# Performance work log

Hardware: AMD Instinct MI355X
Metric: run time of the kernel (lower is better)

Reference implementation:

```python
import jax, jax.numpy as jnp
import numpy as np

B, N, C, H = 4, 4096, 1024, 16
D = C // H


def setup_inputs() -> dict:
    key = jax.random.key(0)
    ks = jax.random.split(key, 15)
    s = 0.02
    f = lambda k, shp: jax.random.normal(k, shp, dtype=jnp.float32) * s
    return {
        "x": f(ks[0], (B, N, C)),
        "qkv_w": f(ks[1], (C, 3 * C)),
        "qkv_b": f(ks[2], (3 * C,)),
        "out_w": f(ks[3], (C, C)),
        "out_b": f(ks[4], (C,)),
        # NB: original code dynamically re-creates position_bias as (1, N, H, H)
        # because q/k/v are never transposed to (B,H,N,D); attention runs over heads.
        "pos_bias": f(ks[5], (1, N, H, H)),
        "conv_w": f(ks[6], (C, C)),
        "conv_b": f(ks[7], (C,)),
        "pw_w": f(ks[8], (C, C, 1)),   # Conv1d kernel_size=1: (out, in, k)
        "pw_b": f(ks[9], (C,)),
        "dw_w": f(ks[10], (C, 1, 3)),  # depthwise Conv1d groups=C: (out, in/groups=1, k)
        "dw_b": f(ks[11], (C,)),
        "tok_w": f(ks[12], (C, C)),
        "tok_b": f(ks[13], (C,)),
    }


def reference(x, qkv_w, qkv_b, out_w, out_b, pos_bias,
              conv_w, conv_b, pw_w, pw_b, dw_w, dw_b, tok_w, tok_b):
    b, n, c = x.shape
    h = pos_bias.shape[2]
    d = c // h
    scale = d ** (-0.5)

    # ---- attention branch (faithful to source: heads axis is attended over) ----
    qkv = (x @ qkv_w + qkv_b).reshape(b, n, h, 3 * d)
    q, k, v = jnp.split(qkv, 3, axis=-1)  # each (B, N, H, D)
    scores = jnp.einsum("bnhd,bngd->bnhg", q, k) * scale + pos_bias  # (B, N, H, H)
    attn_w = jax.nn.softmax(scores, axis=-1)
    attn = jnp.einsum("bnhg,bngd->bnhd", attn_w, v).reshape(b, n, c)
    attn = attn @ out_w + out_b

    # ---- convolutional branch ----
    xc = x @ conv_w + conv_b            # (B, N, C)
    xc = xc.transpose(0, 2, 1)          # (B, C, N)
    dn = ("NCH", "OIH", "NCH")
    xc = jax.lax.conv_general_dilated(xc, pw_w, (1,), [(0, 0)],
                                      dimension_numbers=dn) + pw_b[None, :, None]
    xc = jax.lax.conv_general_dilated(xc, dw_w, (1,), [(1, 1)],
                                      dimension_numbers=dn,
                                      feature_group_count=c) + dw_b[None, :, None]
    xc = xc.transpose(0, 2, 1) @ tok_w + tok_b  # (B, N, C)

    return attn + xc
```

## Files before the change

### kernel.cpp

```cpp
#include <hip/hip_runtime.h>
#include <hip/hip_bf16.h>


typedef __attribute__((ext_vector_type(8))) short sh8;
typedef __attribute__((ext_vector_type(4))) float f4;

__device__ __forceinline__ float bf2f(short s) {
  unsigned u = ((unsigned)(unsigned short)s) << 16;
  return __builtin_bit_cast(float, u);
}
__device__ __forceinline__ short f2bf(float f) {
  return __builtin_bit_cast(short, __float2bfloat16(f));
}
__device__ __forceinline__ void g2l16(const void* g, void* l) {
  __builtin_amdgcn_global_load_lds(
      (const __attribute__((address_space(1))) unsigned int*)g,
      (__attribute__((address_space(3))) unsigned int*)l, 16, 0, 0);
}

__global__ __launch_bounds__(256) void cvt_f32_bf16(
    const float* __restrict__ src, short* __restrict__ dst, int n8) {
  int i = blockIdx.x * 256 + threadIdx.x;
  if (i >= n8) return;
  float4 a = ((const float4*)src)[i * 2];
  float4 b = ((const float4*)src)[i * 2 + 1];
  sh8 o;
  o[0] = f2bf(a.x); o[1] = f2bf(a.y); o[2] = f2bf(a.z); o[3] = f2bf(a.w);
  o[4] = f2bf(b.x); o[5] = f2bf(b.y); o[6] = f2bf(b.z); o[7] = f2bf(b.w);
  ((sh8*)dst)[i] = o;
}

__global__ __launch_bounds__(256) void transpose_f32_bf16(
    const float* __restrict__ src, short* __restrict__ dst,
    int N, int ldd, int coff) {
  __shared__ float tile[32][33];
  int kb = blockIdx.y * 32, nb = blockIdx.x * 32;
  int tx = threadIdx.x, ty = threadIdx.y;
#pragma unroll
  for (int j = 0; j < 32; j += 8)
    tile[ty + j][tx] = src[(size_t)(kb + ty + j) * N + nb + tx];
  __syncthreads();
#pragma unroll
  for (int j = 0; j < 32; j += 8)
    dst[(size_t)(nb + ty + j) * ldd + coff + kb + tx] = f2bf(tile[tx][ty + j]);
}

__global__ __launch_bounds__(256) void prep_misc(
    const float* __restrict__ pw_w, const float* __restrict__ conv_b,
    const float* __restrict__ pw_b, const float* __restrict__ qkv_b,
    const float* __restrict__ out_b, const float* __restrict__ tok_b,
    const float* __restrict__ dw_w, const float* __restrict__ dw_b,
    float* __restrict__ bias4, float* __restrict__ bcat,
    float* __restrict__ dw0, float* __restrict__ dw1,
    float* __restrict__ dw2, float* __restrict__ dwb) {
  int o = blockIdx.x;
  if (o < 1024) {
    float part = 0.f;
    for (int i = threadIdx.x; i < 1024; i += 256)
      part += pw_w[(size_t)o * 1024 + i] * conv_b[i];
#pragma unroll
    for (int off = 32; off >= 1; off >>= 1) part += __shfl_down(part, off);
    __shared__ float red[4];
    int wid = threadIdx.x >> 6, lane = threadIdx.x & 63;
    if (lane == 0) red[wid] = part;
    __syncthreads();
    if (threadIdx.x == 0) {
      float s = red[0] + red[1] + red[2] + red[3];
      bias4[3072 + o] = s + pw_b[o];
      bcat[o] = out_b[o] + tok_b[o];
      dw0[o] = dw_w[o * 3 + 0];
      dw1[o] = dw_w[o * 3 + 1];
      dw2[o] = dw_w[o * 3 + 2];
      dwb[o] = dw_b[o];
    }
  }
  if (threadIdx.x == 0) bias4[o] = qkv_b[o];
}

template <int OUT_BF16>
__global__ __launch_bounds__(256, 2) void gemm128(
    const short* __restrict__ A, const short* __restrict__ Bt,
    void* __restrict__ Cp, const float* __restrict__ bias, int K, int ldc) {
  __shared__ short As[128 * 32];
  __shared__ short Bs[128 * 32];
  const int wid = threadIdx.x >> 6, lane = threadIdx.x & 63;
  const int bm = blockIdx.y, bn = blockIdx.x;
  const int wr = wid >> 1, wc = wid & 1;
  const size_t abase = (size_t)bm * 128 * K;
  const size_t bbase = (size_t)bn * 128 * K;
  const int r16 = lane & 15, ko = (lane >> 4) * 8;

  f4 acc[4][4] = {};

  for (int k0 = 0; k0 < K; k0 += 32) {
    __syncthreads();
#pragma unroll
    for (int c = 0; c < 2; ++c) {
      int ch = c * 256 + wid * 64 + lane;
      int row = ch >> 2, kc = (ch & 3) * 8;
      g2l16(A + abase + (size_t)row * K + k0 + kc, &As[ch * 8]);
      g2l16(Bt + bbase + (size_t)row * K + k0 + kc, &Bs[ch * 8]);
    }
    __syncthreads();
    sh8 af[4], bf[4];
#pragma unroll
    for (int i = 0; i < 4; ++i)
      af[i] = *(const sh8*)&As[(wr * 64 + i * 16 + r16) * 32 + ko];
#pragma unroll
    for (int j = 0; j < 4; ++j)
      bf[j] = *(const sh8*)&Bs[(wc * 64 + j * 16 + r16) * 32 + ko];
#pragma unroll
    for (int i = 0; i < 4; ++i)
#pragma unroll
      for (int j = 0; j < 4; ++j)
        acc[i][j] = __builtin_amdgcn_mfma_f32_16x16x32_bf16(af[i], bf[j],
                                                            acc[i][j], 0, 0, 0);
  }

  const int crow = wr * 64 + (lane >> 4) * 4;
  const int ccol = wc * 64 + r16;
#pragma unroll
  for (int i = 0; i < 4; ++i) {
#pragma unroll
    for (int j = 0; j < 4; ++j) {
      int col = bn * 128 + ccol + j * 16;
      float bv = bias ? bias[col] : 0.f;
#pragma unroll
      for (int r = 0; r < 4; ++r) {
        int row = bm * 128 + crow + i * 16 + r;
        float v = acc[i][j][r] + bv;
        if (OUT_BF16)
          ((short*)Cp)[(size_t)row * ldc + col] = f2bf(v);
        else
          ((float*)Cp)[(size_t)row * ldc + col] = v;
      }
    }
  }
}

template <int OUT_BF16>
__global__ __launch_bounds__(512, 2) void gemm8p(
    const short* __restrict__ A, const short* __restrict__ Bt,
    void* __restrict__ Cp, const float* __restrict__ bias,
    int K, int ldc, int nbn) {
  __shared__ short lds[65536];
  const int tid = threadIdx.x;
  const int lane = tid & 63, wid = tid >> 6;
  const int wr = wid >> 2, wc = wid & 3;
  const int r16 = lane & 15;
  const int kidx = ((lane >> 4) ^ ((r16 >> 1) & 3)) << 3;

  const int cpx = gridDim.x >> 3;
  const int swz = (blockIdx.x & 7) * cpx + (blockIdx.x >> 3);
  const int bm = swz / nbn, bn = swz % nbn;

  const short* Ag = A + (size_t)bm * 256 * K;
  const short* Bg = Bt + (size_t)bn * 256 * K;

  int goff0, goff1, loff0, loff1;
  {
    int s0 = tid, row0 = s0 >> 2;
    int kc0 = (s0 & 3) ^ ((row0 >> 1) & 3);
    goff0 = row0 * K + kc0 * 8;
    loff0 = s0 * 8;
    int s1 = 512 + tid, row1 = s1 >> 2;
    int kc1 = (s1 & 3) ^ ((row1 >> 1) & 3);
    goff1 = row1 * K + kc1 * 8;
    loff1 = s1 * 8;
  }

  f4 acc[8][4] = {};
  const int NT = K >> 6;

#define SOP(GB, DS)                                         \
  do {                                                      \
    g2l16((GB) + goff0, (DS) + loff0);                      \
    g2l16((GB) + goff1, (DS) + loff1);                      \
  } while (0)

  SOP(Ag, &lds[0]);
  SOP(Bg, &lds[16384]);
  SOP(Ag + 32, &lds[8192]);
  SOP(Bg + 32, &lds[24576]);
  SOP(Ag + 64, &lds[32768]);
  SOP(Bg + 64, &lds[32768 + 16384]);
  asm volatile("s_waitcnt vmcnt(6)" ::: "memory");
  __builtin_amdgcn_sched_barrier(0);
  __builtin_amdgcn_s_barrier();
  __builtin_amdgcn_sched_barrier(0);

  for (int t = 0; t < NT; ++t) {
    const int b = t & 1;
    const short* buf = &lds[b * 32768];
    short* bufN = &lds[(b ^ 1) * 32768];
    short* bufC = &lds[b * 32768];
    const int t1 = (t + 1 < NT) ? t + 1 : 0;
    const int t2 = (t + 2 < NT) ? t + 2 : 0;

    sh8 af[8], bfr[4];

#pragma unroll
    for (int i = 0; i < 4; ++i)
      af[i] = *(const sh8*)&buf[(wr * 128 + i * 16 + r16) * 32 + kidx];
#pragma unroll
    for (int j = 0; j < 4; ++j)
      bfr[j] = *(const sh8*)&buf[16384 + (wc * 64 + j * 16 + r16) * 32 + kidx];
    SOP(Ag + t1 * 64 + 32, bufN + 8192);
    asm volatile("s_waitcnt vmcnt(6)" ::: "memory");
    __builtin_amdgcn_sched_barrier(0);
    __builtin_amdgcn_s_barrier();
    __builtin_amdgcn_sched_barrier(0);
    __builtin_amdgcn_s_setprio(1);
#pragma unroll
    for (int i = 0; i < 4; ++i)
#pragma unroll
      for (int j = 0; j < 4; ++j)
        acc[i][j] = __builtin_amdgcn_mfma_f32_16x16x32_bf16(af[i], bfr[j],
                                                            acc[i][j], 0, 0, 0);
    __builtin_amdgcn_s_setprio(0);
    __builtin_amdgcn_sched_barrier(0);
    __builtin_amdgcn_s_barrier();
    __builtin_amdgcn_sched_barrier(0);

#pragma unroll
    for (int i = 4; i < 8; ++i)
      af[i] = *(const sh8*)&buf[(wr * 128 + i * 16 + r16) * 32 + kidx];
    SOP(Bg + t1 * 64 + 32, bufN + 24576);
    asm volatile("s_waitcnt vmcnt(6)" ::: "memory");
    __builtin_amdgcn_sched_barrier(0);
    __builtin_amdgcn_s_barrier();
    __builtin_amdgcn_sched_barrier(0);
    __builtin_amdgcn_s_setprio(1);
#pragma unroll
    for (int i = 4; i < 8; ++i)
#pragma unroll
      for (int j = 0; j < 4; ++j)
        acc[i][j] = __builtin_amdgcn_mfma_f32_16x16x32_bf16(af[i], bfr[j],
                                                            acc[i][j], 0, 0, 0);
    __builtin_amdgcn_s_setprio(0);
    __builtin_amdgcn_sched_barrier(0);
    __builtin_amdgcn_s_barrier();
    __builtin_amdgcn_sched_barrier(0);

#pragma unroll
    for (int i = 0; i < 4; ++i)
      af[i] = *(const sh8*)&buf[8192 + (wr * 128 + i * 16 + r16) * 32 + kidx];
#pragma unroll
    for (int j = 0; j < 4; ++j)
      bfr[j] = *(const sh8*)&buf[24576 + (wc * 64 + j * 16 + r16) * 32 + kidx];
    SOP(Ag + t2 * 64, bufC);
    asm volatile("s_waitcnt vmcnt(6)" ::: "memory");
    __builtin_amdgcn_sched_barrier(0);
    __builtin_amdgcn_s_barrier();
    __builtin_amdgcn_sched_barrier(0);
    __builtin_amdgcn_s_setprio(1);
#pragma unroll
    for (int i = 0; i < 4; ++i)
#pragma unroll
      for (int j = 0; j < 4; ++j)
        acc[i][j] = __builtin_amdgcn_mfma_f32_16x16x32_bf16(af[i], bfr[j],
                                                            acc[i][j], 0, 0, 0);
    __builtin_amdgcn_s_setprio(0);
    __builtin_amdgcn_sched_barrier(0);
    __builtin_amdgcn_s_barrier();
    __builtin_amdgcn_sched_barrier(0);

#pragma unroll
    for (int i = 4; i < 8; ++i)
      af[i] = *(const sh8*)&buf[8192 + (wr * 128 + i * 16 + r16) * 32 + kidx];
    SOP(Bg + t2 * 64, bufC + 16384);
    asm volatile("s_waitcnt vmcnt(6)" ::: "memory");
    __builtin_amdgcn_sched_barrier(0);
    __builtin_amdgcn_s_barrier();
    __builtin_amdgcn_sched_barrier(0);
    __builtin_amdgcn_s_setprio(1);
#pragma unroll
    for (int i = 4; i < 8; ++i)
#pragma unroll
      for (int j = 0; j < 4; ++j)
        acc[i][j] = __builtin_amdgcn_mfma_f32_16x16x32_bf16(af[i], bfr[j],
                                                            acc[i][j], 0, 0, 0);
    __builtin_amdgcn_s_setprio(0);
    __builtin_amdgcn_sched_barrier(0);
    __builtin_amdgcn_s_barrier();
    __builtin_amdgcn_sched_barrier(0);
  }
#undef SOP

  const int crow0 = bm * 256 + wr * 128 + (lane >> 4) * 4;
  const int ccol0 = bn * 256 + wc * 64 + r16;
  float bv[4];
#pragma unroll
  for (int j = 0; j < 4; ++j) bv[j] = bias ? bias[ccol0 + j * 16] : 0.f;
#pragma unroll
  for (int i = 0; i < 8; ++i) {
#pragma unroll
    for (int r = 0; r < 4; ++r) {
      size_t rowoff = (size_t)(crow0 + i * 16 + r) * ldc + ccol0;
#pragma unroll
      for (int j = 0; j < 4; ++j) {
        float v = acc[i][j][r] + bv[j];
        if (OUT_BF16)
          ((short*)Cp)[rowoff + j * 16] = f2bf(v);
        else
          ((float*)Cp)[rowoff + j * 16] = v;
      }
    }
  }
}

__global__ __launch_bounds__(256) void epilogue(
    const short* __restrict__ qkvx, const float* __restrict__ pos_bias,
    const float* __restrict__ dw0, const float* __restrict__ dw1,
    const float* __restrict__ dw2, const float* __restrict__ dwb,
    short* __restrict__ xcat) {
  __shared__ short sq[4 * 3072];
  __shared__ short slice[6 * 1024];
  int t0 = blockIdx.x * 4;
#pragma unroll
  for (int c = 0; c < 6; ++c) {
    int g = c * 256 + threadIdx.x;
    int tok = (g * 683) >> 18;
    int off = g - tok * 384;
    ((sh8*)sq)[tok * 384 + off] =
        *(const sh8*)(qkvx + (size_t)(t0 + tok) * 4096 + off * 8);
  }
#pragma unroll
  for (int s = 0; s < 3; ++s) {
    int g = s * 256 + threadIdx.x;
    int r = g >> 7, off = g & 127;
    int gr = t0 - 1 + r;
    sh8 v = {};
    if (gr >= 0 && gr < 16384)
      v = *(const sh8*)(qkvx + (size_t)gr * 4096 + 3072 + off * 8);
    ((sh8*)slice)[g] = v;
  }
  __syncthreads();

  int wid = threadIdx.x >> 6, lane = threadIdx.x & 63;
  int t = t0 + wid, n = t & 4095;
  int h = lane >> 2, sub = lane & 3;
  const short* base = sq + wid * 3072 + h * 192;

  float qf[64];
#pragma unroll
  for (int c = 0; c < 8; ++c) {
    sh8 v8 = *(const sh8*)(base + c * 8);
#pragma unroll
    for (int j = 0; j < 8; ++j) qf[c * 8 + j] = bf2f(v8[j]);
  }

  const float* pb = pos_bias + (size_t)n * 256 + h * 16 + sub * 4;
  float p[4];
  float m = -1e30f;
#pragma unroll
  for (int g4 = 0; g4 < 4; ++g4) {
    int g = sub * 4 + g4;
    const short* kk = sq + wid * 3072 + g * 192 + 64;
    float acc = 0.f;
#pragma unroll
    for (int c = 0; c < 8; ++c) {
      sh8 k8 = *(const sh8*)(kk + c * 8);
#pragma unroll
      for (int j = 0; j < 8; ++j) acc += qf[c * 8 + j] * bf2f(k8[j]);
    }
    p[g4] = acc * 0.125f + pb[g4];
    m = fmaxf(m, p[g4]);
  }
  m = fmaxf(m, __shfl_xor(m, 1));
  m = fmaxf(m, __shfl_xor(m, 2));
  float sum = 0.f;
#pragma unroll
  for (int g4 = 0; g4 < 4; ++g4) {
    p[g4] = __expf(p[g4] - m);
    sum += p[g4];
  }
  sum += __shfl_xor(sum, 1);
  sum += __shfl_xor(sum, 2);
  float inv = 1.0f / sum;
#pragma unroll
  for (int g4 = 0; g4 < 4; ++g4) p[g4] *= inv;

  float pall[16];
#pragma unroll
  for (int g = 0; g < 16; ++g)
    pall[g] = __shfl(p[g & 3], (lane & 60) | (g >> 2));

  float o[16] = {};
#pragma unroll
  for (int g = 0; g < 16; ++g) {
    const short* vv = sq + wid * 3072 + g * 192 + 128 + sub * 16;
    sh8 va = *(const sh8*)vv;
    sh8 vb = *(const sh8*)(vv + 8);
#pragma unroll
    for (int j = 0; j < 8; ++j) {
      o[j] += pall[g] * bf2f(va[j]);
      o[8 + j] += pall[g] * bf2f(vb[j]);
    }
  }
  sh8 oa, ob;
#pragma unroll
  for (int j = 0; j < 8; ++j) {
    oa[j] = f2bf(o[j]);
    ob[j] = f2bf(o[8 + j]);
  }
  short* dst = xcat + (size_t)t * 2048 + h * 64 + sub * 16;
  *(sh8*)dst = oa;
  *(sh8*)(dst + 8) = ob;

#pragma unroll
  for (int it = 0; it < 2; ++it) {
    int w = it * 256 + threadIdx.x;
    int tok = w >> 7, co = (w & 127) * 8;
    int tt = t0 + tok, nn = tt & 4095;
    const short* lo8 = slice + tok * 1024 + co;
    const short* mi8 = lo8 + 1024;
    const short* hi8 = lo8 + 2048;
    sh8 lo = (nn > 0) ? *(const sh8*)lo8 : sh8{};
    sh8 mi = *(const sh8*)mi8;
    sh8 hi = (nn < 4095) ? *(const sh8*)hi8 : sh8{};
    sh8 out;
#pragma unroll
    for (int j = 0; j < 8; ++j) {
      float v = dw0[co + j] * bf2f(lo[j]) + dw1[co + j] * bf2f(mi[j]) +
                dw2[co + j] * bf2f(hi[j]) + dwb[co + j];
      out[j] = f2bf(v);
    }
    *(sh8*)(xcat + (size_t)tt * 2048 + 1024 + co) = out;
  }
}

extern "C" void kernel_launch(void* const* d_in, const int* in_sizes, int n_in,
                              void* d_out, int out_size, void* d_ws,
                              size_t ws_size, hipStream_t stream) {
  const float* x      = (const float*)d_in[0];
  const float* qkv_w  = (const float*)d_in[1];
  const float* qkv_b  = (const float*)d_in[2];
  const float* out_w  = (const float*)d_in[3];
  const float* out_b  = (const float*)d_in[4];
  const float* pos_b  = (const float*)d_in[5];
  const float* conv_w = (const float*)d_in[6];
  const float* conv_b = (const float*)d_in[7];
  const float* pw_w   = (const float*)d_in[8];
  const float* pw_b   = (const float*)d_in[9];
  const float* dw_w   = (const float*)d_in[10];
  const float* dw_b   = (const float*)d_in[11];
  const float* tok_w  = (const float*)d_in[12];
  const float* tok_b  = (const float*)d_in[13];

  const int M = 16384;
  char* ws = (char*)d_ws;
  size_t off = 0;
  auto alloc = [&](size_t bytes) -> void* {
    void* p = ws + off;
    off += (bytes + 255) & ~(size_t)255;
    return p;
  };
  short* xb    = (short*)alloc((size_t)M * 1024 * 2);
  short* wbig  = (short*)alloc((size_t)4096 * 1024 * 2);
  short* wcatT = (short*)alloc((size_t)1024 * 2048 * 2);
  short* convb = (short*)alloc((size_t)1024 * 1024 * 2);
  short* pwb   = (short*)alloc((size_t)1024 * 1024 * 2);
  short* qkvx  = (short*)alloc((size_t)M * 4096 * 2);
  short* xcat  = (short*)alloc((size_t)M * 2048 * 2);
  float* bias4 = (float*)alloc(4096 * 4);
  float* bcat  = (float*)alloc(1024 * 4);
  float* dw0   = (float*)alloc(1024 * 4);
  float* dw1   = (float*)alloc(1024 * 4);
  float* dw2   = (float*)alloc(1024 * 4);
  float* dwb   = (float*)alloc(1024 * 4);
  (void)ws_size; (void)in_sizes; (void)n_in; (void)out_size;

  cvt_f32_bf16<<<8192, 256, 0, stream>>>(x, xb, M * 1024 / 8);
  cvt_f32_bf16<<<512, 256, 0, stream>>>(conv_w, convb, 1024 * 1024 / 8);
  cvt_f32_bf16<<<512, 256, 0, stream>>>(pw_w, pwb, 1024 * 1024 / 8);
  transpose_f32_bf16<<<dim3(96, 32), dim3(32, 8), 0, stream>>>(qkv_w, wbig, 3072, 1024, 0);
  transpose_f32_bf16<<<dim3(32, 32), dim3(32, 8), 0, stream>>>(out_w, wcatT, 1024, 2048, 0);
  transpose_f32_bf16<<<dim3(32, 32), dim3(32, 8), 0, stream>>>(tok_w, wcatT, 1024, 2048, 1024);
  prep_misc<<<3072, 256, 0, stream>>>(pw_w, conv_b, pw_b, qkv_b, out_b, tok_b,
                                      dw_w, dw_b, bias4, bcat, dw0, dw1, dw2, dwb);
  gemm128<1><<<dim3(8, 8), 256, 0, stream>>>(pwb, convb, wbig + (size_t)3072 * 1024,
                                             nullptr, 1024, 1024);

  gemm8p<1><<<1024, 512, 0, stream>>>(xb, wbig, qkvx, bias4, 1024, 4096, 16);

  epilogue<<<4096, 256, 0, stream>>>(qkvx, pos_b, dw0, dw1, dw2, dwb, xcat);

  gemm8p<0><<<256, 512, 0, stream>>>(xcat, wcatT, d_out, bcat, 2048, 1024, 4);
}
```

Baseline: 331.0 us.

## Merge conversion/transpose launches and restructure gemm8p prefetch wait schedule

Result: no change. 326.4 us (-1.4%).

```diff
diff --git a/kernel.cpp b/kernel.cpp
--- a/kernel.cpp
+++ b/kernel.cpp
@@ -18,16 +18,27 @@
       (__attribute__((address_space(3))) unsigned int*)l, 16, 0, 0);
 }
 
-__global__ __launch_bounds__(256) void cvt_f32_bf16(
-    const float* __restrict__ src, short* __restrict__ dst, int n8) {
+__global__ __launch_bounds__(256) void cvt3(
+    const float* __restrict__ x, const float* __restrict__ conv_w,
+    const float* __restrict__ pw_w, short* __restrict__ xb,
+    short* __restrict__ convb, short* __restrict__ pwb) {
   int i = blockIdx.x * 256 + threadIdx.x;
-  if (i >= n8) return;
-  float4 a = ((const float4*)src)[i * 2];
-  float4 b = ((const float4*)src)[i * 2 + 1];
+  const float* src;
+  short* dst;
+  int off;
+  if (i < 2097152) {
+    src = x; dst = xb; off = i;
+  } else if (i < 2228224) {
+    src = conv_w; dst = convb; off = i - 2097152;
+  } else {
+    src = pw_w; dst = pwb; off = i - 2228224;
+  }
+  float4 a = ((const float4*)src)[off * 2];
+  float4 b = ((const float4*)src)[off * 2 + 1];
   sh8 o;
   o[0] = f2bf(a.x); o[1] = f2bf(a.y); o[2] = f2bf(a.z); o[3] = f2bf(a.w);
   o[4] = f2bf(b.x); o[5] = f2bf(b.y); o[6] = f2bf(b.z); o[7] = f2bf(b.w);
-  ((sh8*)dst)[i] = o;
+  ((sh8*)dst)[off] = o;
 }
 
 __global__ __launch_bounds__(256) void transpose_f32_bf16(
@@ -43,6 +54,23 @@
 #pragma unroll
   for (int j = 0; j < 32; j += 8)
     dst[(size_t)(nb + ty + j) * ldd + coff + kb + tx] = f2bf(tile[tx][ty + j]);
+}
+
+__global__ __launch_bounds__(256) void transpose2(
+    const float* __restrict__ out_w, const float* __restrict__ tok_w,
+    short* __restrict__ dst) {
+  __shared__ float tile[32][33];
+  const float* src = blockIdx.z ? tok_w : out_w;
+  int coff = blockIdx.z ? 1024 : 0;
+  int kb = blockIdx.y * 32, nb = blockIdx.x * 32;
+  int tx = threadIdx.x, ty = threadIdx.y;
+#pragma unroll
+  for (int j = 0; j < 32; j += 8)
+    tile[ty + j][tx] = src[(size_t)(kb + ty + j) * 1024 + nb + tx];
+  __syncthreads();
+#pragma unroll
+  for (int j = 0; j < 32; j += 8)
+    dst[(size_t)(nb + ty + j) * 2048 + coff + kb + tx] = f2bf(tile[tx][ty + j]);
 }
 
 __global__ __launch_bounds__(256) void prep_misc(
@@ -178,22 +206,31 @@
     g2l16((GB) + goff1, (DS) + loff1);                      \
   } while (0)
 
-  SOP(Ag, &lds[0]);
-  SOP(Bg, &lds[16384]);
-  SOP(Ag + 32, &lds[8192]);
-  SOP(Bg + 32, &lds[24576]);
-  SOP(Ag + 64, &lds[32768]);
-  SOP(Bg + 64, &lds[32768 + 16384]);
-  asm volatile("s_waitcnt vmcnt(6)" ::: "memory");
-  __builtin_amdgcn_sched_barrier(0);
-  __builtin_amdgcn_s_barrier();
-  __builtin_amdgcn_sched_barrier(0);
+#define PHASE_SYNC()                                        \
+  do {                                                      \
+    __builtin_amdgcn_sched_barrier(0);                      \
+    __builtin_amdgcn_s_barrier();                           \
+    __builtin_amdgcn_sched_barrier(0);                      \
+  } while (0)
+
+  {
+    short* b0 = &lds[0];
+    short* b1 = &lds[32768];
+    SOP(Ag, b0 + 0);
+    SOP(Bg, b0 + 16384);
+    SOP(Ag + 32, b0 + 8192);
+    SOP(Bg + 32, b0 + 24576);
+    SOP(Bg + 64, b1 + 16384);
+    SOP(Ag + 64, b1 + 0);
+  }
+  asm volatile("s_waitcnt vmcnt(4)" ::: "memory");
+  PHASE_SYNC();
 
   for (int t = 0; t < NT; ++t) {
     const int b = t & 1;
     const short* buf = &lds[b * 32768];
+    short* bufC = &lds[b * 32768];
     short* bufN = &lds[(b ^ 1) * 32768];
-    short* bufC = &lds[b * 32768];
     const int t1 = (t + 1 < NT) ? t + 1 : 0;
     const int t2 = (t + 2 < NT) ? t + 2 : 0;
 
@@ -206,10 +243,8 @@
     for (int j = 0; j < 4; ++j)
       bfr[j] = *(const sh8*)&buf[16384 + (wc * 64 + j * 16 + r16) * 32 + kidx];
     SOP(Ag + t1 * 64 + 32, bufN + 8192);
-    asm volatile("s_waitcnt vmcnt(6)" ::: "memory");
-    __builtin_amdgcn_sched_barrier(0);
-    __builtin_amdgcn_s_barrier();
-    __builtin_amdgcn_sched_barrier(0);
+    SOP(Bg + t1 * 64 + 32, bufN + 24576);
+    PHASE_SYNC();
     __builtin_amdgcn_s_setprio(1);
 #pragma unroll
     for (int i = 0; i < 4; ++i)
@@ -218,18 +253,13 @@
         acc[i][j] = __builtin_amdgcn_mfma_f32_16x16x32_bf16(af[i], bfr[j],
                                                             acc[i][j], 0, 0, 0);
     __builtin_amdgcn_s_setprio(0);
-    __builtin_amdgcn_sched_barrier(0);
-    __builtin_amdgcn_s_barrier();
-    __builtin_amdgcn_sched_barrier(0);
+    PHASE_SYNC();
 
 #pragma unroll
     for (int i = 4; i < 8; ++i)
       af[i] = *(const sh8*)&buf[(wr * 128 + i * 16 + r16) * 32 + kidx];
-    SOP(Bg + t1 * 64 + 32, bufN + 24576);
-    asm volatile("s_waitcnt vmcnt(6)" ::: "memory");
-    __builtin_amdgcn_sched_barrier(0);
-    __builtin_amdgcn_s_barrier();
-    __builtin_amdgcn_sched_barrier(0);
+    SOP(Bg + t2 * 64, bufC + 16384);
+    PHASE_SYNC();
     __builtin_amdgcn_s_setprio(1);
 #pragma unroll
     for (int i = 4; i < 8; ++i)
@@ -238,9 +268,7 @@
         acc[i][j] = __builtin_amdgcn_mfma_f32_16x16x32_bf16(af[i], bfr[j],
                                                             acc[i][j], 0, 0, 0);
     __builtin_amdgcn_s_setprio(0);
-    __builtin_amdgcn_sched_barrier(0);
-    __builtin_amdgcn_s_barrier();
-    __builtin_amdgcn_sched_barrier(0);
+    PHASE_SYNC();
 
 #pragma unroll
     for (int i = 0; i < 4; ++i)
@@ -248,11 +276,8 @@
 #pragma unroll
     for (int j = 0; j < 4; ++j)
       bfr[j] = *(const sh8*)&buf[24576 + (wc * 64 + j * 16 + r16) * 32 + kidx];
-    SOP(Ag + t2 * 64, bufC);
-    asm volatile("s_waitcnt vmcnt(6)" ::: "memory");
-    __builtin_amdgcn_sched_barrier(0);
-    __builtin_amdgcn_s_barrier();
-    __builtin_amdgcn_sched_barrier(0);
+    SOP(Ag + t2 * 64, bufC + 0);
+    PHASE_SYNC();
     __builtin_amdgcn_s_setprio(1);
 #pragma unroll
     for (int i = 0; i < 4; ++i)
@@ -261,18 +286,13 @@
         acc[i][j] = __builtin_amdgcn_mfma_f32_16x16x32_bf16(af[i], bfr[j],
                                                             acc[i][j], 0, 0, 0);
     __builtin_amdgcn_s_setprio(0);
-    __builtin_amdgcn_sched_barrier(0);
-    __builtin_amdgcn_s_barrier();
-    __builtin_amdgcn_sched_barrier(0);
+    PHASE_SYNC();
 
 #pragma unroll
     for (int i = 4; i < 8; ++i)
       af[i] = *(const sh8*)&buf[8192 + (wr * 128 + i * 16 + r16) * 32 + kidx];
-    SOP(Bg + t2 * 64, bufC + 16384);
-    asm volatile("s_waitcnt vmcnt(6)" ::: "memory");
-    __builtin_amdgcn_sched_barrier(0);
-    __builtin_amdgcn_s_barrier();
-    __builtin_amdgcn_sched_barrier(0);
+    asm volatile("s_waitcnt vmcnt(4)" ::: "memory");
+    PHASE_SYNC();
     __builtin_amdgcn_s_setprio(1);
 #pragma unroll
     for (int i = 4; i < 8; ++i)
@@ -281,11 +301,10 @@
         acc[i][j] = __builtin_amdgcn_mfma_f32_16x16x32_bf16(af[i], bfr[j],
                                                             acc[i][j], 0, 0, 0);
     __builtin_amdgcn_s_setprio(0);
-    __builtin_amdgcn_sched_barrier(0);
-    __builtin_amdgcn_s_barrier();
-    __builtin_amdgcn_sched_barrier(0);
+    PHASE_SYNC();
   }
 #undef SOP
+#undef PHASE_SYNC
 
   const int crow0 = bm * 256 + wr * 128 + (lane >> 4) * 4;
   const int ccol0 = bn * 256 + wc * 64 + r16;
@@ -471,12 +490,9 @@
   float* dwb   = (float*)alloc(1024 * 4);
   (void)ws_size; (void)in_sizes; (void)n_in; (void)out_size;
 
-  cvt_f32_bf16<<<8192, 256, 0, stream>>>(x, xb, M * 1024 / 8);
-  cvt_f32_bf16<<<512, 256, 0, stream>>>(conv_w, convb, 1024 * 1024 / 8);
-  cvt_f32_bf16<<<512, 256, 0, stream>>>(pw_w, pwb, 1024 * 1024 / 8);
+  cvt3<<<9216, 256, 0, stream>>>(x, conv_w, pw_w, xb, convb, pwb);
   transpose_f32_bf16<<<dim3(96, 32), dim3(32, 8), 0, stream>>>(qkv_w, wbig, 3072, 1024, 0);
-  transpose_f32_bf16<<<dim3(32, 32), dim3(32, 8), 0, stream>>>(out_w, wcatT, 1024, 2048, 0);
-  transpose_f32_bf16<<<dim3(32, 32), dim3(32, 8), 0, stream>>>(tok_w, wcatT, 1024, 2048, 1024);
+  transpose2<<<dim3(32, 32, 2), dim3(32, 8), 0, stream>>>(out_w, tok_w, wcatT);
   prep_misc<<<3072, 256, 0, stream>>>(pw_w, conv_b, pw_b, qkv_b, out_b, tok_b,
                                       dw_w, dw_b, bias4, bcat, dw0, dw1, dw2, dwb);
   gemm128<1><<<dim3(8, 8), 256, 0, stream>>>(pwb, convb, wbig + (size_t)3072 * 1024,
```
